# Performance work log

Hardware: AMD Instinct MI355X
Metric: run time of the kernel (lower is better)

## Reference

```python
import jax, jax.numpy as jnp
import numpy as np

N = 100000
E = 1600000


def gcn_conv(x, W, b, src, dst, dinv):
    # PyG GCNConv: h = x @ W; symmetric normalization with self-loops;
    # out[i] = sum_{j->i} dinv[j]*dinv[i]*h[j] + dinv[i]^2*h[i] + b
    h = x @ W
    norm = dinv[src] * dinv[dst]                      # [E]
    msg = h[src] * norm[:, None]                      # [E, d] gather
    out = jax.ops.segment_sum(msg, dst, num_segments=N)  # scatter-add
    out = out + h * (dinv * dinv)[:, None]            # self-loop term
    return out + b


def setup_inputs() -> dict:
    key = jax.random.key(0)
    ks = jax.random.split(key, 8)
    nfeat, nhid, nclass = 128, 128, 40
    x = jax.random.normal(ks[0], (N, nfeat), dtype=jnp.float32)
    edge_index = jax.random.randint(ks[1], (2, E), 0, N, dtype=jnp.int64)
    s = 1.0 / np.sqrt(nfeat)
    W0 = jax.random.uniform(ks[2], (nfeat, nhid), jnp.float32, -s, s)
    b0 = jnp.zeros((nhid,), jnp.float32)
    W1 = jax.random.uniform(ks[3], (nhid, nhid), jnp.float32, -s, s)
    b1 = jnp.zeros((nhid,), jnp.float32)
    W2 = jax.random.uniform(ks[4], (nhid, nclass), jnp.float32, -s, s)
    b2 = jnp.zeros((nclass,), jnp.float32)
    return {"x": x, "W0": W0, "b0": b0, "W1": W1, "b1": b1,
            "W2": W2, "b2": b2, "edge_index": edge_index}


def reference(x, W0, b0, W1, b1, W2, b2, edge_index):
    src, dst = edge_index[0], edge_index[1]
    # degree (with self-loop) on destination nodes, symmetric norm
    deg = jax.ops.segment_sum(jnp.ones((E,), jnp.float32), dst, num_segments=N) + 1.0
    dinv = jax.lax.rsqrt(deg)
    h = gcn_conv(x, W0, b0, src, dst, dinv)
    h = jax.nn.relu(h)  # dropout is identity in eval mode
    h = gcn_conv(h, W1, b1, src, dst, dinv)
    h = jax.nn.relu(h)
    out = gcn_conv(h, W2, b2, src, dst, dinv)
    return out
```

## Files before the change

kernel.cpp:

```cpp
#include <hip/hip_runtime.h>
#include <hip/hip_fp16.h>


#define CAP 8192
#define NBMAX 512

typedef _Float16 f16;
typedef __attribute__((ext_vector_type(8))) _Float16 f16x8;
typedef __attribute__((ext_vector_type(4))) _Float16 f16x4;
typedef __attribute__((ext_vector_type(4))) float f32x4;

__global__ __launch_bounds__(256)
void bucket_prep_kernel(const int* __restrict__ src, const int* __restrict__ dst,
                        int E, int gP1, int NB,
                        int* __restrict__ bucket_cnt, unsigned* __restrict__ bucketbuf,
                        const float* __restrict__ W0, const float* __restrict__ W1,
                        const float* __restrict__ W2,
                        __half* __restrict__ w0t, __half* __restrict__ w1t,
                        __half* __restrict__ w2t) {
  int b = blockIdx.x;
  if (b < gP1) {
    __shared__ int hist[NBMAX];
    __shared__ int cbase[NBMAX];
    int tid = threadIdx.x;
    for (int i = tid; i < NB; i += 256) hist[i] = 0;
    __syncthreads();
    int e0 = b * 4096;
    int eend = min(e0 + 4096, E);
    for (int e = e0 + tid; e < eend; e += 256)
      atomicAdd(&hist[((unsigned)dst[e]) >> 8], 1);
    __syncthreads();
    for (int i = tid; i < NB; i += 256) {
      int h = hist[i];
      cbase[i] = h ? atomicAdd(&bucket_cnt[i], h) : 0;
    }
    __syncthreads();
    for (int i = tid; i < NB; i += 256) hist[i] = 0;
    __syncthreads();
    for (int e = e0 + tid; e < eend; e += 256) {
      int d = dst[e];
      int s = src[e];
      int bk = ((unsigned)d) >> 8;
      int idx = cbase[bk] + atomicAdd(&hist[bk], 1);
      if (idx < CAP)
        bucketbuf[(size_t)bk * CAP + idx] = (((unsigned)s) << 8) | (unsigned)(d & 255);
    }
  } else {
    int i = (b - gP1) * 256 + threadIdx.x;
    if (i < 16384) {
      int n = i >> 7, k = i & 127;
      w0t[i] = __float2half_rn(W0[k * 128 + n]);
    } else if (i < 32768) {
      int j = i - 16384;
      int n = j >> 7, k = j & 127;
      w1t[j] = __float2half_rn(W1[k * 128 + n]);
    } else if (i < 38912) {
      int j = i - 32768;
      int n = j >> 7, k = j & 127;
      w2t[j] = (n < 40) ? __float2half_rn(W2[k * 40 + n]) : __float2half_rn(0.f);
    }
  }
}

struct P2Shared {
  unsigned plist[CAP];
  int cnts[256];
  int sm[256];
};

__device__ __forceinline__
void phase2_body(const unsigned* __restrict__ bucketbuf, const int* __restrict__ bucket_cnt,
                 int* __restrict__ rowptr, float* __restrict__ dinv,
                 int* __restrict__ col, int N, int E, int NB, int b, P2Shared& sh) {
  int tid = threadIdx.x;
  int cnt_b = min(bucket_cnt[b], CAP);

  int part = 0;
  for (int i = tid; i < b; i += 256) part += bucket_cnt[i];
  sh.sm[tid] = part;
  __syncthreads();
#pragma unroll
  for (int off = 128; off > 0; off >>= 1) {
    if (tid < off) sh.sm[tid] += sh.sm[tid + off];
    __syncthreads();
  }
  int base = sh.sm[0];
  __syncthreads();

  for (int i = tid; i < cnt_b; i += 256)
    sh.plist[i] = bucketbuf[(size_t)b * CAP + i];
  sh.cnts[tid] = 0;
  __syncthreads();
  for (int i = tid; i < cnt_b; i += 256)
    atomicAdd(&sh.cnts[sh.plist[i] & 255u], 1);
  __syncthreads();

  int myc = sh.cnts[tid];
  sh.sm[tid] = myc;
  __syncthreads();
#pragma unroll
  for (int off = 1; off < 256; off <<= 1) {
    int u = (tid >= off) ? sh.sm[tid - off] : 0;
    __syncthreads();
    sh.sm[tid] += u;
    __syncthreads();
  }
  int exc = sh.sm[tid] - myc;

  int n = (b << 8) + tid;
  if (n < N) {
    rowptr[n] = base + exc;
    dinv[n] = 1.0f / sqrtf((float)myc + 1.0f);
  }
  if (b == NB - 1 && tid == 0) rowptr[N] = E;
  __syncthreads();

  sh.cnts[tid] = base + exc;
  __syncthreads();
  for (int i = tid; i < cnt_b; i += 256) {
    unsigned p = sh.plist[i];
    int pos = atomicAdd(&sh.cnts[p & 255u], 1);
    col[pos] = (int)(p >> 8);
  }
}

template <typename TIN>
__device__ __forceinline__
void mfma_gemm128_body(const TIN* __restrict__ X, const __half* __restrict__ Wt,
                       __half* __restrict__ G, int nrows, int blk,
                       f16 (*xs)[72], f16 (*ws)[72]) {
  const int tid = threadIdx.x;
  const int wave = tid >> 6;
  const int lane = tid & 63;
  const int mrow = lane & 15;
  const int kg = lane >> 4;
  const int row0 = blk * 128;

  f32x4 acc[2][8];
#pragma unroll
  for (int i = 0; i < 2; ++i)
#pragma unroll
    for (int j = 0; j < 8; ++j) acc[i][j] = (f32x4){0.f, 0.f, 0.f, 0.f};

  for (int k0 = 0; k0 < 128; k0 += 64) {
    if constexpr (sizeof(TIN) == 4) {
#pragma unroll
      for (int t = tid; t < 2048; t += 256) {
        int r = t >> 4;
        int kk = (t & 15) * 4;
        float4 v = make_float4(0.f, 0.f, 0.f, 0.f);
        if (row0 + r < nrows)
          v = *(const float4*)((const float*)X + (size_t)(row0 + r) * 128 + k0 + kk);
        f16x4 hv = {(f16)v.x, (f16)v.y, (f16)v.z, (f16)v.w};
        *(f16x4*)&xs[r][kk] = hv;
      }
    } else {
#pragma unroll
      for (int t = tid; t < 1024; t += 256) {
        int r = t >> 3;
        int kk = (t & 7) * 8;
        f16x8 v = (f16x8){0, 0, 0, 0, 0, 0, 0, 0};
        if (row0 + r < nrows)
          v = *(const f16x8*)((const f16*)X + (size_t)(row0 + r) * 128 + k0 + kk);
        *(f16x8*)&xs[r][kk] = v;
      }
    }
#pragma unroll
    for (int t = tid; t < 1024; t += 256) {
      int r = t >> 3;
      int kk = (t & 7) * 8;
      *(f16x8*)&ws[r][kk] =
          *(const f16x8*)((const f16*)Wt + (size_t)r * 128 + k0 + kk);
    }
    __syncthreads();
#pragma unroll
    for (int ks = 0; ks < 64; ks += 32) {
      f16x8 a0 = *(const f16x8*)&xs[wave * 32 + mrow][ks + kg * 8];
      f16x8 a1 = *(const f16x8*)&xs[wave * 32 + 16 + mrow][ks + kg * 8];
#pragma unroll
      for (int nt = 0; nt < 8; ++nt) {
        f16x8 b = *(const f16x8*)&ws[nt * 16 + mrow][ks + kg * 8];
        acc[0][nt] = __builtin_amdgcn_mfma_f32_16x16x32_f16(a0, b, acc[0][nt], 0, 0, 0);
        acc[1][nt] = __builtin_amdgcn_mfma_f32_16x16x32_f16(a1, b, acc[1][nt], 0, 0, 0);
      }
    }
    __syncthreads();
  }
#pragma unroll
  for (int mt = 0; mt < 2; ++mt) {
    int rbase = row0 + wave * 32 + mt * 16 + kg * 4;
#pragma unroll
    for (int i = 0; i < 4; ++i) {
      int grow = rbase + i;
      if (grow < nrows) {
        __half* gp = G + (size_t)grow * 128 + mrow;
#pragma unroll
        for (int nt = 0; nt < 8; ++nt)
          gp[nt * 16] = __float2half_rn(acc[mt][nt][i]);
      }
    }
  }
}

__global__ __launch_bounds__(256)
void mfma_gemm128_kernel(const __half* __restrict__ X, const __half* __restrict__ Wt,
                         __half* __restrict__ G, int nrows) {
  __shared__ f16 xs[128][72];
  __shared__ f16 ws[128][72];
  mfma_gemm128_body<__half>(X, Wt, G, nrows, blockIdx.x, xs, ws);
}

__global__ __launch_bounds__(256)
void gemm128_build_kernel(const float* __restrict__ X, const __half* __restrict__ Wt,
                          __half* __restrict__ G, int nrows, int gGemm,
                          const unsigned* __restrict__ bucketbuf,
                          const int* __restrict__ bucket_cnt,
                          int* __restrict__ rowptr, float* __restrict__ dinv,
                          int* __restrict__ col, int N, int E, int NB) {
  __shared__ char shraw[2 * 128 * 72 * sizeof(f16)];
  if ((int)blockIdx.x < gGemm) {
    f16 (*xs)[72] = (f16(*)[72])shraw;
    f16 (*ws)[72] = (f16(*)[72])(shraw + 128 * 72 * sizeof(f16));
    mfma_gemm128_body<float>(X, Wt, G, nrows, blockIdx.x, xs, ws);
  } else {
    phase2_body(bucketbuf, bucket_cnt, rowptr, dinv, col, N, E, NB,
                blockIdx.x - gGemm, *(P2Shared*)shraw);
  }
}

__global__ __launch_bounds__(256)
void mfma_gemm48_kernel(const __half* __restrict__ X, const __half* __restrict__ Wt,
                        __half* __restrict__ G, int nrows) {
  __shared__ f16 xs[128][72];
  __shared__ f16 ws[48][72];
  const int tid = threadIdx.x;
  const int wave = tid >> 6;
  const int lane = tid & 63;
  const int mrow = lane & 15;
  const int kg = lane >> 4;
  const int row0 = blockIdx.x * 128;

  f32x4 acc[2][3];
#pragma unroll
  for (int i = 0; i < 2; ++i)
#pragma unroll
    for (int j = 0; j < 3; ++j) acc[i][j] = (f32x4){0.f, 0.f, 0.f, 0.f};

  for (int k0 = 0; k0 < 128; k0 += 64) {
#pragma unroll
    for (int t = tid; t < 1024; t += 256) {
      int r = t >> 3;
      int kk = (t & 7) * 8;
      f16x8 v = (f16x8){0, 0, 0, 0, 0, 0, 0, 0};
      if (row0 + r < nrows)
        v = *(const f16x8*)((const f16*)X + (size_t)(row0 + r) * 128 + k0 + kk);
      *(f16x8*)&xs[r][kk] = v;
    }
#pragma unroll
    for (int t = tid; t < 384; t += 256) {
      int r = t >> 3;
      int kk = (t & 7) * 8;
      *(f16x8*)&ws[r][kk] =
          *(const f16x8*)((const f16*)Wt + (size_t)r * 128 + k0 + kk);
    }
    __syncthreads();
#pragma unroll
    for (int ks = 0; ks < 64; ks += 32) {
      f16x8 a0 = *(const f16x8*)&xs[wave * 32 + mrow][ks + kg * 8];
      f16x8 a1 = *(const f16x8*)&xs[wave * 32 + 16 + mrow][ks + kg * 8];
#pragma unroll
      for (int nt = 0; nt < 3; ++nt) {
        f16x8 b = *(const f16x8*)&ws[nt * 16 + mrow][ks + kg * 8];
        acc[0][nt] = __builtin_amdgcn_mfma_f32_16x16x32_f16(a0, b, acc[0][nt], 0, 0, 0);
        acc[1][nt] = __builtin_amdgcn_mfma_f32_16x16x32_f16(a1, b, acc[1][nt], 0, 0, 0);
      }
    }
    __syncthreads();
  }
#pragma unroll
  for (int mt = 0; mt < 2; ++mt) {
    int rbase = row0 + wave * 32 + mt * 16 + kg * 4;
#pragma unroll
    for (int i = 0; i < 4; ++i) {
      int grow = rbase + i;
      if (grow < nrows) {
#pragma unroll
        for (int nt = 0; nt < 3; ++nt) {
          int c = nt * 16 + mrow;
          if (c < 40)
            G[(size_t)grow * 40 + c] = __float2half_rn(acc[mt][nt][i]);
        }
      }
    }
  }
}

template <bool RELU, typename TOUT>
__global__ __launch_bounds__(256)
void aggregate128_kernel(const __half* __restrict__ G, const int* __restrict__ rowptr,
                         const int* __restrict__ col, const float* __restrict__ dinv,
                         const float* __restrict__ bias, TOUT* __restrict__ out,
                         int n) {
  int wid = threadIdx.x >> 6;
  int lane = threadIdx.x & 63;
  int node = blockIdx.x * 4 + wid;
  if (node >= n) return;

  int sub = lane >> 4;
  int c = lane & 15;
  const float4* g4 = (const float4*)G;

  int e = rowptr[node];
  int end = rowptr[node + 1];
  float di = dinv[node];

  float a0 = 0.f, a1 = 0.f, a2 = 0.f, a3 = 0.f,
        a4 = 0.f, a5 = 0.f, a6 = 0.f, a7 = 0.f;

  auto accumw = [&](float4 raw, float w) {
    const __half2* h = (const __half2*)&raw;
    float2 f0 = __half22float2(h[0]);
    float2 f1 = __half22float2(h[1]);
    float2 f2 = __half22float2(h[2]);
    float2 f3 = __half22float2(h[3]);
    a0 = fmaf(w, f0.x, a0); a1 = fmaf(w, f0.y, a1);
    a2 = fmaf(w, f1.x, a2); a3 = fmaf(w, f1.y, a3);
    a4 = fmaf(w, f2.x, a4); a5 = fmaf(w, f2.y, a5);
    a6 = fmaf(w, f3.x, a6); a7 = fmaf(w, f3.y, a7);
  };

  if (sub == 0) accumw(g4[(size_t)node * 16 + c], di);

  int base = e;
  for (; base + 16 <= end; base += 16) {
    int s0 = col[base + sub];
    int s1 = col[base + sub + 4];
    int s2 = col[base + sub + 8];
    int s3 = col[base + sub + 12];
    float w0 = dinv[s0], w1 = dinv[s1], w2 = dinv[s2], w3 = dinv[s3];
    float4 r0 = g4[(size_t)s0 * 16 + c];
    float4 r1 = g4[(size_t)s1 * 16 + c];
    float4 r2 = g4[(size_t)s2 * 16 + c];
    float4 r3 = g4[(size_t)s3 * 16 + c];
    accumw(r0, w0);
    accumw(r1, w1);
    accumw(r2, w2);
    accumw(r3, w3);
  }
  for (; base + 4 <= end; base += 4) {
    int s0 = col[base + sub];
    accumw(g4[(size_t)s0 * 16 + c], dinv[s0]);
  }
  if (base + sub < end) {
    int s0 = col[base + sub];
    accumw(g4[(size_t)s0 * 16 + c], dinv[s0]);
  }

  a0 += __shfl_xor(a0, 16); a1 += __shfl_xor(a1, 16);
  a2 += __shfl_xor(a2, 16); a3 += __shfl_xor(a3, 16);
  a4 += __shfl_xor(a4, 16); a5 += __shfl_xor(a5, 16);
  a6 += __shfl_xor(a6, 16); a7 += __shfl_xor(a7, 16);
  a0 += __shfl_xor(a0, 32); a1 += __shfl_xor(a1, 32);
  a2 += __shfl_xor(a2, 32); a3 += __shfl_xor(a3, 32);
  a4 += __shfl_xor(a4, 32); a5 += __shfl_xor(a5, 32);
  a6 += __shfl_xor(a6, 32); a7 += __shfl_xor(a7, 32);

  if (sub == 0) {
    const float4* b4 = (const float4*)bias;
    float4 bb0 = b4[c * 2];
    float4 bb1 = b4[c * 2 + 1];
    float o[8] = {di * a0 + bb0.x, di * a1 + bb0.y, di * a2 + bb0.z,
                  di * a3 + bb0.w, di * a4 + bb1.x, di * a5 + bb1.y,
                  di * a6 + bb1.z, di * a7 + bb1.w};
    if (RELU) {
#pragma unroll
      for (int j = 0; j < 8; ++j) o[j] = fmaxf(o[j], 0.f);
    }
    if constexpr (sizeof(TOUT) == 2) {
      union { __half2 h[4]; float4 f; } u;
      u.h[0] = __floats2half2_rn(o[0], o[1]);
      u.h[1] = __floats2half2_rn(o[2], o[3]);
      u.h[2] = __floats2half2_rn(o[4], o[5]);
      u.h[3] = __floats2half2_rn(o[6], o[7]);
      *(float4*)((__half*)out + (size_t)node * 128 + c * 8) = u.f;
    } else {
      float4* op = (float4*)((float*)out + (size_t)node * 128 + c * 8);
      op[0] = make_float4(o[0], o[1], o[2], o[3]);
      op[1] = make_float4(o[4], o[5], o[6], o[7]);
    }
  }
}

__global__ __launch_bounds__(256)
void aggregate40_kernel(const __half* __restrict__ G, const int* __restrict__ rowptr,
                        const int* __restrict__ col, const float* __restrict__ dinv,
                        const float* __restrict__ bias, float* __restrict__ out,
                        int n) {
  int wid = threadIdx.x >> 6;
  int lane = threadIdx.x & 63;
  int node = blockIdx.x * 4 + wid;
  if (node >= n) return;

  int sub = lane / 10;
  int c = lane % 10;
  const float2* g2 = (const float2*)G;

  int e = rowptr[node];
  int end = rowptr[node + 1];
  float di = dinv[node];

  float ax = 0.f, ay = 0.f, az = 0.f, aw = 0.f;
  if (sub == 0) {
    float2 raw = g2[(size_t)node * 10 + c];
    float2 f0 = __half22float2(*(const __half2*)&raw.x);
    float2 f1 = __half22float2(*(const __half2*)&raw.y);
    ax = di * f0.x; ay = di * f0.y; az = di * f1.x; aw = di * f1.y;
  }

  if (sub < 6) {
    int i = e + sub;
    for (; i + 11 < end; i += 12) {
      int s0 = col[i];
      int s1 = col[i + 6];
      float w0 = dinv[s0], w1 = dinv[s1];
      float2 r0 = g2[(size_t)s0 * 10 + c];
      float2 r1 = g2[(size_t)s1 * 10 + c];
      float2 f0 = __half22float2(*(const __half2*)&r0.x);
      float2 f1 = __half22float2(*(const __half2*)&r0.y);
      float2 f2 = __half22float2(*(const __half2*)&r1.x);
      float2 f3 = __half22float2(*(const __half2*)&r1.y);
      ax = fmaf(w0, f0.x, fmaf(w1, f2.x, ax));
      ay = fmaf(w0, f0.y, fmaf(w1, f2.y, ay));
      az = fmaf(w0, f1.x, fmaf(w1, f3.x, az));
      aw = fmaf(w0, f1.y, fmaf(w1, f3.y, aw));
    }
    for (; i < end; i += 6) {
      int s0 = col[i];
      float w0 = dinv[s0];
      float2 r0 = g2[(size_t)s0 * 10 + c];
      float2 f0 = __half22float2(*(const __half2*)&r0.x);
      float2 f1 = __half22float2(*(const __half2*)&r0.y);
      ax = fmaf(w0, f0.x, ax); ay = fmaf(w0, f0.y, ay);
      az = fmaf(w0, f1.x, az); aw = fmaf(w0, f1.y, aw);
    }
  }

  float bx = __shfl(ax, lane + 30), by = __shfl(ay, lane + 30),
        bz = __shfl(az, lane + 30), bw = __shfl(aw, lane + 30);
  ax += bx; ay += by; az += bz; aw += bw;
  float c1x = __shfl(ax, lane + 10), c1y = __shfl(ay, lane + 10),
        c1z = __shfl(az, lane + 10), c1w = __shfl(aw, lane + 10);
  float c2x = __shfl(ax, lane + 20), c2y = __shfl(ay, lane + 20),
        c2z = __shfl(az, lane + 20), c2w = __shfl(aw, lane + 20);

  if (sub == 0) {
    float sx = ax + c1x + c2x;
    float sy = ay + c1y + c2y;
    float sz = az + c1z + c2z;
    float sw = aw + c1w + c2w;
    float4 bb = ((const float4*)bias)[c];
    float4 o = make_float4(di * sx + bb.x, di * sy + bb.y, di * sz + bb.z,
                           di * sw + bb.w);
    ((float4*)out)[(size_t)node * 10 + c] = o;
  }
}

extern "C" void kernel_launch(void* const* d_in, const int* in_sizes, int n_in,
                              void* d_out, int out_size, void* d_ws, size_t ws_size,
                              hipStream_t stream) {
  const float* x = (const float*)d_in[0];
  const float* W0 = (const float*)d_in[1];
  const float* b0 = (const float*)d_in[2];
  const float* W1 = (const float*)d_in[3];
  const float* b1 = (const float*)d_in[4];
  const float* W2 = (const float*)d_in[5];
  const float* b2 = (const float*)d_in[6];
  const int* ei = (const int*)d_in[7];

  const int N = in_sizes[0] / 128;
  const int E = in_sizes[7] / 2;
  const int* src = ei;
  const int* dst = ei + E;
  const int NB = (N + 255) >> 8;

  char* w = (char*)d_ws;
  size_t off = 0;
  auto alloc = [&](size_t bytes) -> void* {
    void* p = w + off;
    off = (off + bytes + 255) & ~(size_t)255;
    return p;
  };
  int* bucket_cnt = (int*)alloc((size_t)NBMAX * 4);
  float* dinv = (float*)alloc((size_t)N * 4);
  int* rowptr = (int*)alloc((size_t)(N + 1) * 4);
  int* col = (int*)alloc((size_t)E * 4);
  unsigned* bucketbuf = (unsigned*)alloc((size_t)NB * CAP * 4);
  __half* gbuf = (__half*)alloc((size_t)N * 128 * 2);
  __half* hbuf = (__half*)alloc((size_t)N * 128 * 2);
  __half* w0t = (__half*)alloc(128 * 128 * 2);
  __half* w1t = (__half*)alloc(128 * 128 * 2);
  __half* w2t = (__half*)alloc(48 * 128 * 2);
  (void)ws_size;

  hipMemsetAsync(bucket_cnt, 0, (size_t)NBMAX * 4, stream);

  dim3 blk(256);
  int gP1 = (E + 4095) / 4096;
  int gW = (38912 + 255) / 256;
  int gGemm = (N + 127) / 128;
  int gAgg = (N + 3) / 4;

  bucket_prep_kernel<<<gP1 + gW, blk, 0, stream>>>(src, dst, E, gP1, NB,
                                                   bucket_cnt, bucketbuf,
                                                   W0, W1, W2, w0t, w1t, w2t);
  gemm128_build_kernel<<<gGemm + NB, blk, 0, stream>>>(x, w0t, gbuf, N, gGemm,
                                                       bucketbuf, bucket_cnt,
                                                       rowptr, dinv, col, N, E, NB);

  aggregate128_kernel<true, __half><<<gAgg, blk, 0, stream>>>(gbuf, rowptr, col, dinv,
                                                              b0, hbuf, N);
  mfma_gemm128_kernel<<<gGemm, blk, 0, stream>>>(hbuf, w1t, gbuf, N);
  aggregate128_kernel<true, __half><<<gAgg, blk, 0, stream>>>(gbuf, rowptr, col, dinv,
                                                              b1, hbuf, N);
  mfma_gemm48_kernel<<<gGemm, blk, 0, stream>>>(hbuf, w2t, gbuf, N);
  aggregate40_kernel<<<gAgg, blk, 0, stream>>>(gbuf, rowptr, col, dinv, b2,
                                               (float*)d_out, N);
}
```

Measured before the change: 358.3 us.

## Pre-scale GEMM outputs by dinv and software-pipeline edge index loads in aggregation

For layers 2 and 3 the GEMM epilogue now multiplies each output row by dinv[row], so the aggregation kernels no longer gather dinv[src] per edge and sum rows unweighted. The aggregation loops are restructured so each sub-group handles contiguous edges with the next block's column indices prefetched (clamped to E-1), replacing the remainder loops with predicated loads. This removes per-edge random dinv reads and hides col-load latency, at the cost of extra clamped index loads and some wasted iterations on low-degree nodes.

```diff
diff --git a/kernel.cpp b/kernel.cpp
--- a/kernel.cpp
+++ b/kernel.cpp
@@ -124,11 +124,11 @@
   }
 }
 
-template <typename TIN>
+template <typename TIN, bool SCALE>
 __device__ __forceinline__
 void mfma_gemm128_body(const TIN* __restrict__ X, const __half* __restrict__ Wt,
-                       __half* __restrict__ G, int nrows, int blk,
-                       f16 (*xs)[72], f16 (*ws)[72]) {
+                       const float* __restrict__ dinv, __half* __restrict__ G,
+                       int nrows, int blk, f16 (*xs)[72], f16 (*ws)[72]) {
   const int tid = threadIdx.x;
   const int wave = tid >> 6;
   const int lane = tid & 63;
@@ -193,10 +193,11 @@
     for (int i = 0; i < 4; ++i) {
       int grow = rbase + i;
       if (grow < nrows) {
+        float s = SCALE ? dinv[grow] : 1.0f;
         __half* gp = G + (size_t)grow * 128 + mrow;
 #pragma unroll
         for (int nt = 0; nt < 8; ++nt)
-          gp[nt * 16] = __float2half_rn(acc[mt][nt][i]);
+          gp[nt * 16] = __float2half_rn(s * acc[mt][nt][i]);
       }
     }
   }
@@ -204,10 +205,11 @@
 
 __global__ __launch_bounds__(256)
 void mfma_gemm128_kernel(const __half* __restrict__ X, const __half* __restrict__ Wt,
-                         __half* __restrict__ G, int nrows) {
+                         const float* __restrict__ dinv, __half* __restrict__ G,
+                         int nrows) {
   __shared__ f16 xs[128][72];
   __shared__ f16 ws[128][72];
-  mfma_gemm128_body<__half>(X, Wt, G, nrows, blockIdx.x, xs, ws);
+  mfma_gemm128_body<__half, true>(X, Wt, dinv, G, nrows, blockIdx.x, xs, ws);
 }
 
 __global__ __launch_bounds__(256)
@@ -221,7 +223,7 @@
   if ((int)blockIdx.x < gGemm) {
     f16 (*xs)[72] = (f16(*)[72])shraw;
     f16 (*ws)[72] = (f16(*)[72])(shraw + 128 * 72 * sizeof(f16));
-    mfma_gemm128_body<float>(X, Wt, G, nrows, blockIdx.x, xs, ws);
+    mfma_gemm128_body<float, false>(X, Wt, nullptr, G, nrows, blockIdx.x, xs, ws);
   } else {
     phase2_body(bucketbuf, bucket_cnt, rowptr, dinv, col, N, E, NB,
                 blockIdx.x - gGemm, *(P2Shared*)shraw);
@@ -230,7 +232,8 @@
 
 __global__ __launch_bounds__(256)
 void mfma_gemm48_kernel(const __half* __restrict__ X, const __half* __restrict__ Wt,
-                        __half* __restrict__ G, int nrows) {
+                        const float* __restrict__ dinv, __half* __restrict__ G,
+                        int nrows) {
   __shared__ f16 xs[128][72];
   __shared__ f16 ws[48][72];
   const int tid = threadIdx.x;
@@ -284,23 +287,24 @@
     for (int i = 0; i < 4; ++i) {
       int grow = rbase + i;
       if (grow < nrows) {
+        float s = dinv[grow];
 #pragma unroll
         for (int nt = 0; nt < 3; ++nt) {
           int c = nt * 16 + mrow;
           if (c < 40)
-            G[(size_t)grow * 40 + c] = __float2half_rn(acc[mt][nt][i]);
+            G[(size_t)grow * 40 + c] = __float2half_rn(s * acc[mt][nt][i]);
         }
       }
     }
   }
 }
 
-template <bool RELU, typename TOUT>
+template <bool RELU, bool WEIGHTED, typename TOUT>
 __global__ __launch_bounds__(256)
 void aggregate128_kernel(const __half* __restrict__ G, const int* __restrict__ rowptr,
                          const int* __restrict__ col, const float* __restrict__ dinv,
                          const float* __restrict__ bias, TOUT* __restrict__ out,
-                         int n) {
+                         int n, int Em1) {
   int wid = threadIdx.x >> 6;
   int lane = threadIdx.x & 63;
   int node = blockIdx.x * 4 + wid;
@@ -329,31 +333,37 @@
     a6 = fmaf(w, f3.x, a6); a7 = fmaf(w, f3.y, a7);
   };
 
-  if (sub == 0) accumw(g4[(size_t)node * 16 + c], di);
+  if (sub == 0)
+    accumw(g4[(size_t)node * 16 + c], WEIGHTED ? di : 1.0f);
 
   int base = e;
-  for (; base + 16 <= end; base += 16) {
-    int s0 = col[base + sub];
-    int s1 = col[base + sub + 4];
-    int s2 = col[base + sub + 8];
-    int s3 = col[base + sub + 12];
-    float w0 = dinv[s0], w1 = dinv[s1], w2 = dinv[s2], w3 = dinv[s3];
-    float4 r0 = g4[(size_t)s0 * 16 + c];
-    float4 r1 = g4[(size_t)s1 * 16 + c];
-    float4 r2 = g4[(size_t)s2 * 16 + c];
-    float4 r3 = g4[(size_t)s3 * 16 + c];
+  int i0 = base + sub * 4;
+  int s0 = col[min(i0, Em1)];
+  int s1 = col[min(i0 + 1, Em1)];
+  int s2 = col[min(i0 + 2, Em1)];
+  int s3 = col[min(i0 + 3, Em1)];
+
+  while (base < end) {
+    int ii = base + sub * 4;
+    float4 z = make_float4(0.f, 0.f, 0.f, 0.f);
+    float4 r0 = z, r1 = z, r2 = z, r3 = z;
+    if (ii < end)     r0 = g4[(size_t)s0 * 16 + c];
+    if (ii + 1 < end) r1 = g4[(size_t)s1 * 16 + c];
+    if (ii + 2 < end) r2 = g4[(size_t)s2 * 16 + c];
+    if (ii + 3 < end) r3 = g4[(size_t)s3 * 16 + c];
+    float w0 = 1.f, w1 = 1.f, w2 = 1.f, w3 = 1.f;
+    if (WEIGHTED) { w0 = dinv[s0]; w1 = dinv[s1]; w2 = dinv[s2]; w3 = dinv[s3]; }
+    base += 16;
+    int ni = base + sub * 4;
+    int t0 = col[min(ni, Em1)];
+    int t1 = col[min(ni + 1, Em1)];
+    int t2 = col[min(ni + 2, Em1)];
+    int t3 = col[min(ni + 3, Em1)];
     accumw(r0, w0);
     accumw(r1, w1);
     accumw(r2, w2);
     accumw(r3, w3);
-  }
-  for (; base + 4 <= end; base += 4) {
-    int s0 = col[base + sub];
-    accumw(g4[(size_t)s0 * 16 + c], dinv[s0]);
-  }
-  if (base + sub < end) {
-    int s0 = col[base + sub];
-    accumw(g4[(size_t)s0 * 16 + c], dinv[s0]);
+    s0 = t0; s1 = t1; s2 = t2; s3 = t3;
   }
 
   a0 += __shfl_xor(a0, 16); a1 += __shfl_xor(a1, 16);
@@ -395,7 +405,7 @@
 void aggregate40_kernel(const __half* __restrict__ G, const int* __restrict__ rowptr,
                         const int* __restrict__ col, const float* __restrict__ dinv,
                         const float* __restrict__ bias, float* __restrict__ out,
-                        int n) {
+                        int n, int Em1) {
   int wid = threadIdx.x >> 6;
   int lane = threadIdx.x & 63;
   int node = blockIdx.x * 4 + wid;
@@ -403,6 +413,7 @@
 
   int sub = lane / 10;
   int c = lane % 10;
+  bool act = sub < 6;
   const float2* g2 = (const float2*)G;
 
   int e = rowptr[node];
@@ -410,39 +421,31 @@
   float di = dinv[node];
 
   float ax = 0.f, ay = 0.f, az = 0.f, aw = 0.f;
-  if (sub == 0) {
-    float2 raw = g2[(size_t)node * 10 + c];
+  auto acc2 = [&](float2 raw) {
     float2 f0 = __half22float2(*(const __half2*)&raw.x);
     float2 f1 = __half22float2(*(const __half2*)&raw.y);
-    ax = di * f0.x; ay = di * f0.y; az = di * f1.x; aw = di * f1.y;
-  }
-
-  if (sub < 6) {
-    int i = e + sub;
-    for (; i + 11 < end; i += 12) {
-      int s0 = col[i];
-      int s1 = col[i + 6];
-      float w0 = dinv[s0], w1 = dinv[s1];
-      float2 r0 = g2[(size_t)s0 * 10 + c];
-      float2 r1 = g2[(size_t)s1 * 10 + c];
-      float2 f0 = __half22float2(*(const __half2*)&r0.x);
-      float2 f1 = __half22float2(*(const __half2*)&r0.y);
-      float2 f2 = __half22float2(*(const __half2*)&r1.x);
-      float2 f3 = __half22float2(*(const __half2*)&r1.y);
-      ax = fmaf(w0, f0.x, fmaf(w1, f2.x, ax));
-      ay = fmaf(w0, f0.y, fmaf(w1, f2.y, ay));
-      az = fmaf(w0, f1.x, fmaf(w1, f3.x, az));
-      aw = fmaf(w0, f1.y, fmaf(w1, f3.y, aw));
-    }
-    for (; i < end; i += 6) {
-      int s0 = col[i];
-      float w0 = dinv[s0];
-      float2 r0 = g2[(size_t)s0 * 10 + c];
-      float2 f0 = __half22float2(*(const __half2*)&r0.x);
-      float2 f1 = __half22float2(*(const __half2*)&r0.y);
-      ax = fmaf(w0, f0.x, ax); ay = fmaf(w0, f0.y, ay);
-      az = fmaf(w0, f1.x, az); aw = fmaf(w0, f1.y, aw);
-    }
+    ax += f0.x; ay += f0.y; az += f1.x; aw += f1.y;
+  };
+  if (lane < 10) acc2(g2[(size_t)node * 10 + c]);
+
+  int base = e;
+  int i0 = base + sub * 2;
+  int s0 = col[min(i0, Em1)];
+  int s1 = col[min(i0 + 1, Em1)];
+
+  while (base < end) {
+    int ii = base + sub * 2;
+    float2 z = make_float2(0.f, 0.f);
+    float2 r0 = z, r1 = z;
+    if (act && ii < end)     r0 = g2[(size_t)s0 * 10 + c];
+    if (act && ii + 1 < end) r1 = g2[(size_t)s1 * 10 + c];
+    base += 12;
+    int ni = base + sub * 2;
+    int t0 = col[min(ni, Em1)];
+    int t1 = col[min(ni + 1, Em1)];
+    acc2(r0);
+    acc2(r1);
+    s0 = t0; s1 = t1;
   }
 
   float bx = __shfl(ax, lane + 30), by = __shfl(ay, lane + 30),
@@ -453,7 +456,7 @@
   float c2x = __shfl(ax, lane + 20), c2y = __shfl(ay, lane + 20),
         c2z = __shfl(az, lane + 20), c2w = __shfl(aw, lane + 20);
 
-  if (sub == 0) {
+  if (lane < 10) {
     float sx = ax + c1x + c2x;
     float sy = ay + c1y + c2y;
     float sz = az + c1z + c2z;
@@ -517,12 +520,12 @@
                                                        bucketbuf, bucket_cnt,
                                                        rowptr, dinv, col, N, E, NB);
 
-  aggregate128_kernel<true, __half><<<gAgg, blk, 0, stream>>>(gbuf, rowptr, col, dinv,
-                                                              b0, hbuf, N);
-  mfma_gemm128_kernel<<<gGemm, blk, 0, stream>>>(hbuf, w1t, gbuf, N);
-  aggregate128_kernel<true, __half><<<gAgg, blk, 0, stream>>>(gbuf, rowptr, col, dinv,
-                                                              b1, hbuf, N);
-  mfma_gemm48_kernel<<<gGemm, blk, 0, stream>>>(hbuf, w2t, gbuf, N);
+  aggregate128_kernel<true, true, __half><<<gAgg, blk, 0, stream>>>(
+      gbuf, rowptr, col, dinv, b0, hbuf, N, E - 1);
+  mfma_gemm128_kernel<<<gGemm, blk, 0, stream>>>(hbuf, w1t, dinv, gbuf, N);
+  aggregate128_kernel<true, false, __half><<<gAgg, blk, 0, stream>>>(
+      gbuf, rowptr, col, dinv, b1, hbuf, N, E - 1);
+  mfma_gemm48_kernel<<<gGemm, blk, 0, stream>>>(hbuf, w2t, dinv, gbuf, N);
   aggregate40_kernel<<<gAgg, blk, 0, stream>>>(gbuf, rowptr, col, dinv, b2,
-                                               (float*)d_out, N);
-}
+                                               (float*)d_out, N, E - 1);
+}
```

Result: no change. 365.0 us (+1.9%).
